# Kernel optimization log

Measured on AMD Instinct MI355X. Metric: run time of the kernel, lower is better.

The kernel has to match this reference:

```python
import jax, jax.numpy as jnp
import numpy as np

D = 768

def setup_inputs() -> dict:
    key = jax.random.key(0)
    k1, k2, k3, k4, k5 = jax.random.split(key, 5)
    query = jax.random.normal(k1, (32, 1024, D), dtype=jnp.float32)
    key_t = jax.random.normal(k2, (32, 1024, D), dtype=jnp.float32)
    w1 = jax.random.normal(k3, (1, D), dtype=jnp.float32) * 0.02
    w2 = jax.random.normal(k4, (1, D), dtype=jnp.float32) * 0.02
    w3 = jax.random.normal(k5, (1, D), dtype=jnp.float32) * 0.02
    return {"query": query, "key": key_t, "w1": w1, "w2": w2, "w3": w3}

def reference(query, key, w1, w2, w3):
    # q_logit: [B, Lq, 1], k_logit: [B, Lk, 1] -> transposed to [B, 1, Lk]
    q_logit = query @ w1[0]                       # [B, Lq]
    k_logit = key @ w2[0]                         # [B, Lk]
    dot_logit = jnp.einsum('bqd,bkd->bqk', query, w3[0] * key)  # [B, Lq, Lk]
    return q_logit[:, :, None] + k_logit[:, None, :] + dot_logit
```

## Files before the change

kernel.cpp:

```cpp
#include <hip/hip_runtime.h>
#include <hip/hip_bf16.h>

#define BB 32
#define LL 1024
#define DD 768

typedef short bf16x8 __attribute__((ext_vector_type(8)));
typedef float f32x4 __attribute__((ext_vector_type(4)));

__device__ __forceinline__ unsigned short f2bf(float f) {
    unsigned u = __builtin_bit_cast(unsigned, f);
    u += 0x7fffu + ((u >> 16) & 1u);
    return (unsigned short)(u >> 16);
}

__global__ __launch_bounds__(256) void convert_kernel(
    const float* __restrict__ Q, const float* __restrict__ K,
    const float* __restrict__ w1, const float* __restrict__ w2,
    const float* __restrict__ w3,
    unsigned short* __restrict__ Qb, unsigned short* __restrict__ Kb,
    float* __restrict__ qlog, float* __restrict__ klog)
{
    __shared__ __align__(16) float wsh[3 * DD];
    const int tid = threadIdx.x;
    #pragma unroll
    for (int r = 0; r < 3; ++r) {
        const int i = tid + r * 256;
        if (i < 576) {
            float4 v;
            if      (i < 192) v = ((const float4*)w1)[i];
            else if (i < 384) v = ((const float4*)w2)[i - 192];
            else              v = ((const float4*)w3)[i - 384];
            ((float4*)wsh)[i] = v;
        }
    }
    __syncthreads();

    const int ln  = tid & 63;
    const int row = blockIdx.x * 4 + (tid >> 6);
    const size_t base = (size_t)row * DD;
    const float4* wv = (const float4*)wsh;

    float qdot = 0.f, kdot = 0.f;
    #pragma unroll
    for (int c = 0; c < 3; ++c) {
        const int idx = c * 64 + ln;
        float4 qv  = ((const float4*)(Q + base))[idx];
        float4 kv  = ((const float4*)(K + base))[idx];
        float4 w1v = wv[idx];
        float4 w2v = wv[192 + idx];
        float4 w3v = wv[384 + idx];

        qdot += qv.x*w1v.x + qv.y*w1v.y + qv.z*w1v.z + qv.w*w1v.w;
        kdot += kv.x*w2v.x + kv.y*w2v.y + kv.z*w2v.z + kv.w*w2v.w;

        ushort4 pq, pk;
        pq.x = f2bf(qv.x); pq.y = f2bf(qv.y); pq.z = f2bf(qv.z); pq.w = f2bf(qv.w);
        pk.x = f2bf(kv.x * w3v.x); pk.y = f2bf(kv.y * w3v.y);
        pk.z = f2bf(kv.z * w3v.z); pk.w = f2bf(kv.w * w3v.w);
        ((ushort4*)(Qb + base))[idx] = pq;
        ((ushort4*)(Kb + base))[idx] = pk;
    }

    #pragma unroll
    for (int off = 32; off > 0; off >>= 1) {
        qdot += __shfl_down(qdot, off, 64);
        kdot += __shfl_down(kdot, off, 64);
    }
    if (ln == 0) { qlog[row] = qdot; klog[row] = kdot; }
}

__global__ __launch_bounds__(512, 2) void trilinear_gemm(
    const unsigned short* __restrict__ Qb, const unsigned short* __restrict__ Kb,
    const float* __restrict__ qlog, const float* __restrict__ klog,
    float* __restrict__ out)
{
    __shared__ __align__(16) unsigned short As[4][256 * 32];
    __shared__ __align__(16) unsigned short Bs[4][256 * 32];

    const int tid  = threadIdx.x;
    const int w    = tid >> 6, lane = tid & 63;
    const int wq   = w >> 2, wk = w & 3;

    const int id = blockIdx.x;
    const int g  = id & 7;
    const int j  = id >> 3;
    const int b  = g + ((j >> 4) << 3);
    const int t0 = j & 15;
    const int qt = t0 >> 2, kt = t0 & 3;

    const unsigned short* Ag = Qb + ((size_t)b * LL + qt * 256) * DD;
    const unsigned short* Bg = Kb + ((size_t)b * LL + kt * 256) * DD;

    const int srow  = lane >> 2;
    const int scol  = ((lane & 3) ^ ((lane >> 3) & 3)) * 8;
    const int m    = lane & 15;
    const int l    = lane >> 4;
    const int p8   = (l ^ ((m >> 1) & 3)) * 8;

    f32x4 acc[8][4] = {};

    #define STAGE(kt_, s_) do {                                                  \
        const int k0_ = (kt_) * 32;                                              \
        _Pragma("unroll")                                                        \
        for (int j2 = 0; j2 < 2; ++j2) {                                         \
            const int rb_ = j2 * 128 + w * 16;        \
            __builtin_amdgcn_global_load_lds(                                    \
                (const __attribute__((address_space(1))) void*)                  \
                    (Ag + (size_t)(rb_ + srow) * DD + k0_ + scol),               \
                (__attribute__((address_space(3))) void*)&As[s_][rb_ * 32],      \
                16, 0, 0);                                                       \
            __builtin_amdgcn_global_load_lds(                                    \
                (const __attribute__((address_space(1))) void*)                  \
                    (Bg + (size_t)(rb_ + srow) * DD + k0_ + scol),               \
                (__attribute__((address_space(3))) void*)&Bs[s_][rb_ * 32],      \
                16, 0, 0);                                                       \
        }                                                                        \
    } while (0)

    #define COMPUTE(s_) do {                                                     \
        const unsigned short* A_ = As[s_];                                       \
        const unsigned short* B_ = Bs[s_];                                       \
        bf16x8 av[8], bv[4];                                                     \
        _Pragma("unroll")                                                        \
        for (int tt = 0; tt < 8; ++tt)                                           \
            av[tt] = *(const bf16x8*)&A_[(wq * 128 + tt * 16 + m) * 32 + p8];    \
        _Pragma("unroll")                                                        \
        for (int tt = 0; tt < 4; ++tt)                                           \
            bv[tt] = *(const bf16x8*)&B_[(wk * 64 + tt * 16 + m) * 32 + p8];     \
        asm volatile("s_waitcnt lgkmcnt(0)" ::: "memory");                       \
        __builtin_amdgcn_sched_barrier(0);                                       \
        __builtin_amdgcn_s_setprio(1);                                           \
        _Pragma("unroll")                                                        \
        for (int at = 0; at < 8; ++at)                                           \
            _Pragma("unroll")                                                    \
            for (int bt = 0; bt < 4; ++bt)                                       \
                acc[at][bt] = __builtin_amdgcn_mfma_f32_16x16x32_bf16(           \
                    av[at], bv[bt], acc[at][bt], 0, 0, 0);                       \
        __builtin_amdgcn_s_setprio(0);                                           \
    } while (0)

    const int NT = DD / 32;

    STAGE(0, 0);
    STAGE(1, 1);
    STAGE(2, 2);
    asm volatile("s_waitcnt vmcnt(8)" ::: "memory");
    __builtin_amdgcn_s_barrier();
    __builtin_amdgcn_sched_barrier(0);

    int bc = 0, bs = 3;
    for (int t = 0; t < NT - 3; ++t) {
        STAGE(t + 3, bs);
        COMPUTE(bc);
        asm volatile("s_waitcnt vmcnt(8)" ::: "memory");
        __builtin_amdgcn_s_barrier();
        __builtin_amdgcn_sched_barrier(0);
        bc = (bc + 1) & 3;
        bs = (bs + 1) & 3;
    }
    COMPUTE(bc);
    asm volatile("s_waitcnt vmcnt(4)" ::: "memory");
    __builtin_amdgcn_s_barrier();
    __builtin_amdgcn_sched_barrier(0);
    bc = (bc + 1) & 3;
    COMPUTE(bc);
    asm volatile("s_waitcnt vmcnt(0)" ::: "memory");
    __builtin_amdgcn_s_barrier();
    __builtin_amdgcn_sched_barrier(0);
    bc = (bc + 1) & 3;
    COMPUTE(bc);

    #undef STAGE
    #undef COMPUTE

    const int qrow0 = qt * 256 + wq * 128;
    const int kcol0 = kt * 256 + wk * 64;
    const float* ql = qlog + b * LL + qrow0;
    const float* kl = klog + b * LL + kcol0;
    float* outp = out + ((size_t)b * LL + qrow0) * LL + kcol0;
    const int col = lane & 15, r4 = (lane >> 4) * 4;

    #pragma unroll
    for (int at = 0; at < 8; ++at) {
        #pragma unroll
        for (int bt = 0; bt < 4; ++bt) {
            const float klv = kl[bt * 16 + col];
            #pragma unroll
            for (int r = 0; r < 4; ++r) {
                const int row = at * 16 + r4 + r;
                outp[(size_t)row * LL + bt * 16 + col] = acc[at][bt][r] + ql[row] + klv;
            }
        }
    }
}

extern "C" void kernel_launch(void* const* d_in, const int* in_sizes, int n_in,
                              void* d_out, int out_size, void* d_ws, size_t ws_size,
                              hipStream_t stream) {
    const float* Q  = (const float*)d_in[0];
    const float* K  = (const float*)d_in[1];
    const float* w1 = (const float*)d_in[2];
    const float* w2 = (const float*)d_in[3];
    const float* w3 = (const float*)d_in[4];
    float* out = (float*)d_out;

    unsigned short* Qb = (unsigned short*)d_ws;
    unsigned short* Kb = Qb + (size_t)BB * LL * DD;
    float* qlog = (float*)(Kb + (size_t)BB * LL * DD);
    float* klog = qlog + BB * LL;

    convert_kernel<<<BB * LL / 4, 256, 0, stream>>>(Q, K, w1, w2, w3, Qb, Kb, qlog, klog);
    trilinear_gemm<<<512, 512, 0, stream>>>(Qb, Kb, qlog, klog, out);
}
```

Measured before the change: 360.4 us.

## Fuse bf16 conversion and logit dot products into the trilinear GEMM

Removes the separate convert kernel and the bf16 workspace. Each GEMM block now loads fp32 Q and K tiles into registers, computes the w1/w2 logit partial sums, scales K by w3, packs to bf16 and writes swizzled LDS. The pipeline changes from 4-stage async global-to-LDS loads to register-staged double buffering with one-tile-ahead prefetch. This saves the intermediate write/read and a launch, but re-reads fp32 inputs and redoes conversion for every tile sharing the rows.

Result: no change. 365.7 us (+1.5%).

```diff
diff --git a/kernel.cpp b/kernel.cpp
--- a/kernel.cpp
+++ b/kernel.cpp
@@ -8,75 +8,25 @@
 typedef short bf16x8 __attribute__((ext_vector_type(8)));
 typedef float f32x4 __attribute__((ext_vector_type(4)));
 
-__device__ __forceinline__ unsigned short f2bf(float f) {
+__device__ __forceinline__ unsigned f2bf_u(float f) {
     unsigned u = __builtin_bit_cast(unsigned, f);
     u += 0x7fffu + ((u >> 16) & 1u);
-    return (unsigned short)(u >> 16);
+    return u >> 16;
+}
+__device__ __forceinline__ unsigned pack_bf16(float lo, float hi) {
+    return f2bf_u(lo) | (f2bf_u(hi) << 16);
 }
 
-__global__ __launch_bounds__(256) void convert_kernel(
+__global__ __launch_bounds__(512, 2) void trilinear_fused(
     const float* __restrict__ Q, const float* __restrict__ K,
     const float* __restrict__ w1, const float* __restrict__ w2,
     const float* __restrict__ w3,
-    unsigned short* __restrict__ Qb, unsigned short* __restrict__ Kb,
-    float* __restrict__ qlog, float* __restrict__ klog)
-{
-    __shared__ __align__(16) float wsh[3 * DD];
-    const int tid = threadIdx.x;
-    #pragma unroll
-    for (int r = 0; r < 3; ++r) {
-        const int i = tid + r * 256;
-        if (i < 576) {
-            float4 v;
-            if      (i < 192) v = ((const float4*)w1)[i];
-            else if (i < 384) v = ((const float4*)w2)[i - 192];
-            else              v = ((const float4*)w3)[i - 384];
-            ((float4*)wsh)[i] = v;
-        }
-    }
-    __syncthreads();
-
-    const int ln  = tid & 63;
-    const int row = blockIdx.x * 4 + (tid >> 6);
-    const size_t base = (size_t)row * DD;
-    const float4* wv = (const float4*)wsh;
-
-    float qdot = 0.f, kdot = 0.f;
-    #pragma unroll
-    for (int c = 0; c < 3; ++c) {
-        const int idx = c * 64 + ln;
-        float4 qv  = ((const float4*)(Q + base))[idx];
-        float4 kv  = ((const float4*)(K + base))[idx];
-        float4 w1v = wv[idx];
-        float4 w2v = wv[192 + idx];
-        float4 w3v = wv[384 + idx];
-
-        qdot += qv.x*w1v.x + qv.y*w1v.y + qv.z*w1v.z + qv.w*w1v.w;
-        kdot += kv.x*w2v.x + kv.y*w2v.y + kv.z*w2v.z + kv.w*w2v.w;
-
-        ushort4 pq, pk;
-        pq.x = f2bf(qv.x); pq.y = f2bf(qv.y); pq.z = f2bf(qv.z); pq.w = f2bf(qv.w);
-        pk.x = f2bf(kv.x * w3v.x); pk.y = f2bf(kv.y * w3v.y);
-        pk.z = f2bf(kv.z * w3v.z); pk.w = f2bf(kv.w * w3v.w);
-        ((ushort4*)(Qb + base))[idx] = pq;
-        ((ushort4*)(Kb + base))[idx] = pk;
-    }
-
-    #pragma unroll
-    for (int off = 32; off > 0; off >>= 1) {
-        qdot += __shfl_down(qdot, off, 64);
-        kdot += __shfl_down(kdot, off, 64);
-    }
-    if (ln == 0) { qlog[row] = qdot; klog[row] = kdot; }
-}
-
-__global__ __launch_bounds__(512, 2) void trilinear_gemm(
-    const unsigned short* __restrict__ Qb, const unsigned short* __restrict__ Kb,
-    const float* __restrict__ qlog, const float* __restrict__ klog,
     float* __restrict__ out)
 {
-    __shared__ __align__(16) unsigned short As[4][256 * 32];
-    __shared__ __align__(16) unsigned short Bs[4][256 * 32];
+    __shared__ __align__(16) unsigned short As[2][256 * 32];
+    __shared__ __align__(16) unsigned short Bs[2][256 * 32];
+    __shared__ float redq[512], redk[512];
+    __shared__ float qls[256], kls[256];
 
     const int tid  = threadIdx.x;
     const int w    = tid >> 6, lane = tid & 63;
@@ -89,33 +39,59 @@
     const int t0 = j & 15;
     const int qt = t0 >> 2, kt = t0 & 3;
 
-    const unsigned short* Ag = Qb + ((size_t)b * LL + qt * 256) * DD;
-    const unsigned short* Bg = Kb + ((size_t)b * LL + kt * 256) * DD;
+    const float* Qg = Q + ((size_t)b * LL + qt * 256) * DD;
+    const float* Kg = K + ((size_t)b * LL + kt * 256) * DD;
 
-    const int srow  = lane >> 2;
-    const int scol  = ((lane & 3) ^ ((lane >> 3) & 3)) * 8;
+    const int sr = tid & 255;
+    const int hh = __builtin_amdgcn_readfirstlane(tid >> 8);
     const int m    = lane & 15;
     const int l    = lane >> 4;
     const int p8   = (l ^ ((m >> 1) & 3)) * 8;
 
     f32x4 acc[8][4] = {};
+    float4 qf[4], kf[4];
+    float qdot = 0.f, kdot = 0.f;
 
-    #define STAGE(kt_, s_) do {                                                  \
-        const int k0_ = (kt_) * 32;                                              \
+    #define STAGE_LOAD(kt_) do {                                                 \
+        const float* aq_ = Qg + (size_t)sr * DD + (kt_) * 32 + hh * 16;          \
+        const float* bk_ = Kg + (size_t)sr * DD + (kt_) * 32 + hh * 16;          \
         _Pragma("unroll")                                                        \
-        for (int j2 = 0; j2 < 2; ++j2) {                                         \
-            const int rb_ = j2 * 128 + w * 16;        \
-            __builtin_amdgcn_global_load_lds(                                    \
-                (const __attribute__((address_space(1))) void*)                  \
-                    (Ag + (size_t)(rb_ + srow) * DD + k0_ + scol),               \
-                (__attribute__((address_space(3))) void*)&As[s_][rb_ * 32],      \
-                16, 0, 0);                                                       \
-            __builtin_amdgcn_global_load_lds(                                    \
-                (const __attribute__((address_space(1))) void*)                  \
-                    (Bg + (size_t)(rb_ + srow) * DD + k0_ + scol),               \
-                (__attribute__((address_space(3))) void*)&Bs[s_][rb_ * 32],      \
-                16, 0, 0);                                                       \
+        for (int j_ = 0; j_ < 4; ++j_) {                                         \
+            qf[j_] = ((const float4*)aq_)[j_];                                   \
+            kf[j_] = ((const float4*)bk_)[j_];                                   \
         }                                                                        \
+    } while (0)
+
+    #define STAGE_WRITE(kt_, s_) do {                                            \
+        const int k0_ = (kt_) * 32 + hh * 16;                                    \
+        unsigned qa_[8], kb_[8];                                                 \
+        _Pragma("unroll")                                                        \
+        for (int j_ = 0; j_ < 4; ++j_) {                                         \
+            const float4 q_ = qf[j_], k_ = kf[j_];                               \
+            const float a0 = w1[k0_ + 4*j_ + 0], a1 = w1[k0_ + 4*j_ + 1],        \
+                        a2 = w1[k0_ + 4*j_ + 2], a3 = w1[k0_ + 4*j_ + 3];        \
+            const float b0 = w2[k0_ + 4*j_ + 0], b1 = w2[k0_ + 4*j_ + 1],        \
+                        b2 = w2[k0_ + 4*j_ + 2], b3 = w2[k0_ + 4*j_ + 3];        \
+            const float c0 = w3[k0_ + 4*j_ + 0], c1 = w3[k0_ + 4*j_ + 1],        \
+                        c2 = w3[k0_ + 4*j_ + 2], c3 = w3[k0_ + 4*j_ + 3];        \
+            qdot += q_.x*a0 + q_.y*a1 + q_.z*a2 + q_.w*a3;                       \
+            kdot += k_.x*b0 + k_.y*b1 + k_.z*b2 + k_.w*b3;                       \
+            qa_[2*j_    ] = pack_bf16(q_.x, q_.y);                               \
+            qa_[2*j_ + 1] = pack_bf16(q_.z, q_.w);                               \
+            kb_[2*j_    ] = pack_bf16(k_.x * c0, k_.y * c1);                     \
+            kb_[2*j_ + 1] = pack_bf16(k_.z * c2, k_.w * c3);                     \
+        }                                                                        \
+        const int x_ = (sr >> 1) & 3;                                            \
+        unsigned short* ar_ = &As[s_][sr * 32];                                  \
+        unsigned short* br_ = &Bs[s_][sr * 32];                                  \
+        uint4 vq0 = {qa_[0], qa_[1], qa_[2], qa_[3]};                            \
+        uint4 vq1 = {qa_[4], qa_[5], qa_[6], qa_[7]};                            \
+        uint4 vk0 = {kb_[0], kb_[1], kb_[2], kb_[3]};                            \
+        uint4 vk1 = {kb_[4], kb_[5], kb_[6], kb_[7]};                            \
+        *(uint4*)&ar_[((2*hh    ) ^ x_) * 8] = vq0;                              \
+        *(uint4*)&ar_[((2*hh + 1) ^ x_) * 8] = vq1;                              \
+        *(uint4*)&br_[((2*hh    ) ^ x_) * 8] = vk0;                              \
+        *(uint4*)&br_[((2*hh + 1) ^ x_) * 8] = vk1;                              \
     } while (0)
 
     #define COMPUTE(s_) do {                                                     \
@@ -142,42 +118,38 @@
 
     const int NT = DD / 32;
 
-    STAGE(0, 0);
-    STAGE(1, 1);
-    STAGE(2, 2);
-    asm volatile("s_waitcnt vmcnt(8)" ::: "memory");
+    STAGE_LOAD(0);
+    STAGE_WRITE(0, 0);
+    STAGE_LOAD(1);
+    asm volatile("s_waitcnt lgkmcnt(0)" ::: "memory");
     __builtin_amdgcn_s_barrier();
     __builtin_amdgcn_sched_barrier(0);
 
-    int bc = 0, bs = 3;
-    for (int t = 0; t < NT - 3; ++t) {
-        STAGE(t + 3, bs);
-        COMPUTE(bc);
-        asm volatile("s_waitcnt vmcnt(8)" ::: "memory");
+    for (int t = 0; t < NT - 1; ++t) {
+        COMPUTE(t & 1);
+        STAGE_WRITE(t + 1, (t + 1) & 1);
+        if (t + 2 < NT) STAGE_LOAD(t + 2);
+        asm volatile("s_waitcnt lgkmcnt(0)" ::: "memory");
         __builtin_amdgcn_s_barrier();
         __builtin_amdgcn_sched_barrier(0);
-        bc = (bc + 1) & 3;
-        bs = (bs + 1) & 3;
     }
-    COMPUTE(bc);
-    asm volatile("s_waitcnt vmcnt(4)" ::: "memory");
-    __builtin_amdgcn_s_barrier();
-    __builtin_amdgcn_sched_barrier(0);
-    bc = (bc + 1) & 3;
-    COMPUTE(bc);
-    asm volatile("s_waitcnt vmcnt(0)" ::: "memory");
-    __builtin_amdgcn_s_barrier();
-    __builtin_amdgcn_sched_barrier(0);
-    bc = (bc + 1) & 3;
-    COMPUTE(bc);
+    COMPUTE((NT - 1) & 1);
 
-    #undef STAGE
+    #undef STAGE_LOAD
+    #undef STAGE_WRITE
     #undef COMPUTE
+
+    redq[tid] = qdot;
+    redk[tid] = kdot;
+    __syncthreads();
+    if (tid < 256) {
+        qls[tid] = redq[tid] + redq[tid + 256];
+        kls[tid] = redk[tid] + redk[tid + 256];
+    }
+    __syncthreads();
 
     const int qrow0 = qt * 256 + wq * 128;
     const int kcol0 = kt * 256 + wk * 64;
-    const float* ql = qlog + b * LL + qrow0;
-    const float* kl = klog + b * LL + kcol0;
     float* outp = out + ((size_t)b * LL + qrow0) * LL + kcol0;
     const int col = lane & 15, r4 = (lane >> 4) * 4;
 
@@ -185,11 +157,12 @@
     for (int at = 0; at < 8; ++at) {
         #pragma unroll
         for (int bt = 0; bt < 4; ++bt) {
-            const float klv = kl[bt * 16 + col];
+            const float klv = kls[wk * 64 + bt * 16 + col];
             #pragma unroll
             for (int r = 0; r < 4; ++r) {
                 const int row = at * 16 + r4 + r;
-                outp[(size_t)row * LL + bt * 16 + col] = acc[at][bt][r] + ql[row] + klv;
+                outp[(size_t)row * LL + bt * 16 + col] =
+                    acc[at][bt][r] + qls[wq * 128 + row] + klv;
             }
         }
     }
@@ -205,11 +178,7 @@
     const float* w3 = (const float*)d_in[4];
     float* out = (float*)d_out;
 
-    unsigned short* Qb = (unsigned short*)d_ws;
-    unsigned short* Kb = Qb + (size_t)BB * LL * DD;
-    float* qlog = (float*)(Kb + (size_t)BB * LL * DD);
-    float* klog = qlog + BB * LL;
+    (void)d_ws; (void)ws_size;
 
-    convert_kernel<<<BB * LL / 4, 256, 0, stream>>>(Q, K, w1, w2, w3, Qb, Kb, qlog, klog);
-    trilinear_gemm<<<512, 512, 0, stream>>>(Qb, Kb, qlog, klog, out);
+    trilinear_fused<<<512, 512, 0, stream>>>(Q, K, w1, w2, w3, out);
 }
```
